# Kernel optimization log

Measured on AMD Instinct MI355X. Metric: run time of the kernel, lower is better.

Reference implementation:

```python
import jax, jax.numpy as jnp
import numpy as np

BN, N, FIN, FO, H = 4, 2048, 128, 64, 4
D = FO * H  # 256


def setup_inputs() -> dict:
    key = jax.random.key(0)
    ks = jax.random.split(key, 13)
    rnd = lambda k, s, sc=1.0: jax.random.normal(k, s, dtype=jnp.float32) * sc
    return {
        "x": rnd(ks[0], (BN, N, FIN)),
        "adj": rnd(ks[1], (BN, N, N)),
        "W_proj": rnd(ks[2], (D, FIN), 0.08),        # xavier-ish scale
        "score_src": rnd(ks[3], (H, FO), 0.1),        # (head_num, out_features)
        "score_tgt": rnd(ks[4], (H, FO), 0.1),
        "bias_out": jnp.zeros((D,), jnp.float32),
        "w_r": rnd(ks[5], (D, D), 0.06),
        "u_r": rnd(ks[6], (D, D), 0.06),
        "w_z": rnd(ks[7], (D, D), 0.06),
        "b_wz": jnp.full((D,), -2.0, jnp.float32),    # GRUGate init_bias
        "u_z": rnd(ks[8], (D, D), 0.06),
        "w_g": rnd(ks[9], (D, D), 0.06),
        "u_g": rnd(ks[10], (D, D), 0.06),
    }


def reference(x, adj, W_proj, score_src, score_tgt, bias_out,
              w_r, u_r, w_z, b_wz, u_z, w_g, u_g):
    bn, n = x.shape[:2]
    h, fo = score_src.shape
    # eval mode: dropout is identity
    proj_flat = x @ W_proj.T                                   # (bn, n, fo*h)
    # reshape splits last dim as (fo, h): head index fastest-varying
    proj = proj_flat.reshape(bn, n, fo, h).transpose(0, 3, 1, 2)  # (bn, h, n, fo)
    residual = proj_flat                                       # (bn, n, fo*h)
    s_src = jnp.einsum('bhnf,hf->bhn', proj, score_src)
    s_tgt = jnp.einsum('bhnf,hf->bhn', proj, score_tgt)
    scores = jax.nn.leaky_relu(s_src[..., :, None] + s_tgt[..., None, :], 0.2)
    scores = scores + adj[:, None]                             # (bn, h, n, n)
    attn = jax.nn.softmax(scores, axis=-1)
    out = jnp.einsum('bhij,bhjf->bhif', attn, proj)            # (bn, h, n, fo)
    out = out.transpose(0, 2, 1, 3).reshape(bn, n, h * fo)
    # GRUGate is computed in the torch source but its result is discarded
    z = jax.nn.sigmoid(out @ w_z.T + b_wz + residual @ u_z.T)
    r = jax.nn.sigmoid(out @ w_r.T + residual @ u_r.T)
    h_hat = jnp.tanh(out @ w_g.T + (r * residual) @ u_g.T)
    _gru = (1.0 - z) * residual + z * h_hat  # unused, matches source bug
    return jax.nn.elu(out + bias_out)
```

## Files before the change

### kernel.cpp

```cpp
#include <hip/hip_runtime.h>
#include <hip/hip_bf16.h>
#include <math.h>

#define BN_   4
#define NN_   2048
#define FIN_  128
#define FO_   64
#define H_    4
#define D_    256

typedef __attribute__((ext_vector_type(8))) short bf16x8;
typedef __attribute__((ext_vector_type(4))) float floatx4;

#define LOG2E 1.4426950408889634f

#if __has_builtin(__builtin_amdgcn_exp2f)
#define EXP2(x) __builtin_amdgcn_exp2f(x)
#else
#define EXP2(x) exp2f(x)
#endif

__device__ __forceinline__ float bf2f(short u) {
    union { unsigned int i; float f; } v;
    v.i = ((unsigned int)(unsigned short)u) << 16;
    return v.f;
}
__device__ __forceinline__ short f2bf(float f) {
    union { float f; unsigned int u; } v; v.f = f;
    unsigned int r = v.u + 0x7fffu + ((v.u >> 16) & 1u);
    return (short)(unsigned short)(r >> 16);
}

#if defined(__BF16_MANT_DIG__)
typedef __bf16 bfr2 __attribute__((ext_vector_type(2)));
__device__ __forceinline__ unsigned int pack_bf16(float a, float b) {
    union { bfr2 h; unsigned int u; } v;
    v.h = (bfr2){(__bf16)a, (__bf16)b};
    return v.u;
}
#else
__device__ __forceinline__ unsigned int pack_bf16(float a, float b) {
    return ((unsigned int)(unsigned short)f2bf(a)) |
           (((unsigned int)(unsigned short)f2bf(b)) << 16);
}
#endif

__device__ __forceinline__ bf16x8 load8f(const float* __restrict__ p) {
    floatx4 a = *(const floatx4*)p;
    floatx4 b = *(const floatx4*)(p + 4);
    union { bf16x8 v; unsigned int u[4]; } r;
    r.u[0] = pack_bf16(a[0], a[1]);
    r.u[1] = pack_bf16(a[2], a[3]);
    r.u[2] = pack_bf16(b[0], b[1]);
    r.u[3] = pack_bf16(b[2], b[3]);
    return r.v;
}

__device__ __forceinline__ float score_exp(float ssv, float stv, float av) {
    float s = ssv + stv;
    s = fmaxf(s, 0.2f * s);
    return EXP2((s + av) * LOG2E);
}

__global__ __launch_bounds__(256) void proj_kernel(
    const float* __restrict__ x,
    const float* __restrict__ wproj,
    const float* __restrict__ ssrc,
    const float* __restrict__ stgt,
    short* __restrict__ pt,
    float* __restrict__ sS,
    float* __restrict__ sT,
    int b0)
{
    const int tid  = threadIdx.x;
    const int wave = tid >> 6;
    const int lane = tid & 63;
    const int l16  = lane & 15;
    const int quad = lane >> 4;

    const int b_rel = blockIdx.z;
    const int b  = b0 + b_rel;
    const int h  = blockIdx.y;
    const int d0 = h * 64;
    const int j0 = blockIdx.x * 256 + wave * 64;

    floatx4 acc[4][4];
#pragma unroll
    for (int mi = 0; mi < 4; ++mi)
#pragma unroll
        for (int nj = 0; nj < 4; ++nj)
            acc[mi][nj] = (floatx4){0.f, 0.f, 0.f, 0.f};

#pragma unroll
    for (int kc = 0; kc < 4; ++kc) {
        const int c = kc * 32 + quad * 8;
        bf16x8 afr[4], bfr[4];
#pragma unroll
        for (int mi = 0; mi < 4; ++mi) {
            int f = (d0 + mi * 16 + l16) & 63;
            int srow = f * H_ + h;
            afr[mi] = load8f(wproj + srow * FIN_ + c);
        }
#pragma unroll
        for (int nj = 0; nj < 4; ++nj) {
            int j = j0 + nj * 16 + l16;
            bfr[nj] = load8f(x + ((size_t)b * NN_ + j) * FIN_ + c);
        }
#pragma unroll
        for (int mi = 0; mi < 4; ++mi)
#pragma unroll
            for (int nj = 0; nj < 4; ++nj)
                acc[mi][nj] = __builtin_amdgcn_mfma_f32_16x16x32_bf16(
                    afr[mi], bfr[nj], acc[mi][nj], 0, 0, 0);
    }

    const size_t hbase = ((size_t)b_rel * H_ + h) * (size_t)(64 * 2048);
    const int jt0 = j0 >> 5;
#pragma unroll
    for (int mi = 0; mi < 4; ++mi) {
#pragma unroll
        for (int r = 0; r < 4; ++r) {
            const int f15 = quad * 4 + r;
#pragma unroll
            for (int nj = 0; nj < 4; ++nj) {
                const int tile = jt0 + (nj >> 1);
                const int jsub = (nj & 1) * 2 + (l16 >> 3);
                pt[hbase + (size_t)tile * 2048 + mi * 512 + jsub * 128
                   + f15 * 8 + (l16 & 7)] = f2bf(acc[mi][nj][r]);
            }
        }
    }

    float wsv[4][4], wtv[4][4];
#pragma unroll
    for (int mi = 0; mi < 4; ++mi)
#pragma unroll
        for (int r = 0; r < 4; ++r) {
            int f = mi * 16 + quad * 4 + r;
            wsv[mi][r] = ssrc[h * FO_ + f];
            wtv[mi][r] = stgt[h * FO_ + f];
        }
    const size_t sbase = ((size_t)b_rel * H_ + h) * NN_;
#pragma unroll
    for (int nj = 0; nj < 4; ++nj) {
        float ps = 0.f, pg = 0.f;
#pragma unroll
        for (int mi = 0; mi < 4; ++mi)
#pragma unroll
            for (int r = 0; r < 4; ++r) {
                ps = fmaf(wsv[mi][r], acc[mi][nj][r], ps);
                pg = fmaf(wtv[mi][r], acc[mi][nj][r], pg);
            }
        ps += __shfl_xor(ps, 16, 64); ps += __shfl_xor(ps, 32, 64);
        pg += __shfl_xor(pg, 16, 64); pg += __shfl_xor(pg, 32, 64);
        if (quad == 0) {
            int j = j0 + nj * 16 + l16;
            sS[sbase + j] = ps;
            sT[sbase + j] = pg;
        }
    }
}

#define RSTRIDE 65
#define WSLOT   (RSTRIDE * 16 + 16)

__global__ __launch_bounds__(512, 2) void attn_kernel(
    const float* __restrict__ adj,
    const short* __restrict__ pt,
    const float* __restrict__ sS,
    const float* __restrict__ sT,
    const float* __restrict__ bias,
    float* __restrict__ out,
    int b0)
{
    __shared__ union {
        struct {
            float adjs[8][16][36];
            float st[8][4][256];
        } m;
        float red[8][WSLOT];
    } sm;

    const int tid  = threadIdx.x;
    const int w    = tid >> 6;
    const int lane = tid & 63;
    const int l16  = lane & 15;
    const int quad = lane >> 4;
    const int r8   = lane >> 3;
    const int c4   = (lane & 7) * 4;

    const int b_rel = blockIdx.z;
    const int b  = b0 + b_rel;
    const int i0 = blockIdx.x * 16;

    const short* pt2_b = pt + (size_t)b_rel * H_ * (size_t)(64 * 2048);
    const size_t sb = (size_t)b_rel * H_ * NN_;

    {
        const int t = lane * 4;
#pragma unroll
        for (int h = 0; h < 4; ++h)
            *(floatx4*)&sm.m.st[w][h][t] =
                *(const floatx4*)&sT[sb + (size_t)h * NN_ + w * 256 + t];
    }

    float ssv[4];
#pragma unroll
    for (int h = 0; h < 4; ++h)
        ssv[h] = sS[sb + (size_t)h * NN_ + i0 + l16];

    const float* adj_base = adj + ((size_t)b * NN_ + i0) * NN_ + w * 256;

    floatx4 acc[4][4];
#pragma unroll
    for (int h = 0; h < 4; ++h)
#pragma unroll
        for (int K = 0; K < 4; ++K)
            acc[h][K] = (floatx4){0.f, 0.f, 0.f, 0.f};
    float ls[4] = {0.f, 0.f, 0.f, 0.f};

    floatx4 areg0 = *(const floatx4*)(adj_base + (size_t)r8 * NN_ + c4);
    floatx4 areg1 = *(const floatx4*)(adj_base + (size_t)(8 + r8) * NN_ + c4);
    *(floatx4*)&sm.m.adjs[w][r8][c4]     = areg0;
    *(floatx4*)&sm.m.adjs[w][8 + r8][c4] = areg1;

    const int lo8 = lane * 8;

#pragma unroll
    for (int jt = 0; jt < 8; ++jt) {
        const int o  = jt * 32;
        const int qo = quad * 8;

        if (jt < 7) {
            areg0 = *(const floatx4*)(adj_base + (size_t)r8 * NN_ + o + 32 + c4);
            areg1 = *(const floatx4*)(adj_base + (size_t)(8 + r8) * NN_ + o + 32 + c4);
        }

        floatx4 ajA = *(const floatx4*)&sm.m.adjs[w][l16][qo];
        floatx4 ajB = *(const floatx4*)&sm.m.adjs[w][l16][qo + 4];

#pragma unroll
        for (int u = 0; u < 4; ++u) {
            const short* fb = pt2_b + ((size_t)u * 64 + (w * 8 + jt)) * 2048 + lo8;
            bf16x8 bfr[4];
#pragma unroll
            for (int K = 0; K < 4; ++K)
                bfr[K] = *(const bf16x8*)(fb + K * 512);

            const float* stp = &sm.m.st[w][u][qo];
            floatx4 stA = *(const floatx4*)(stp + o);
            floatx4 stB = *(const floatx4*)(stp + o + 4);

            float w0 = score_exp(ssv[u], stA[0], ajA[0]);
            float w1 = score_exp(ssv[u], stA[1], ajA[1]);
            float w2 = score_exp(ssv[u], stA[2], ajA[2]);
            float w3 = score_exp(ssv[u], stA[3], ajA[3]);
            float w4 = score_exp(ssv[u], stB[0], ajB[0]);
            float w5 = score_exp(ssv[u], stB[1], ajB[1]);
            float w6 = score_exp(ssv[u], stB[2], ajB[2]);
            float w7 = score_exp(ssv[u], stB[3], ajB[3]);
            ls[u] += ((w0 + w1) + (w2 + w3)) + ((w4 + w5) + (w6 + w7));
            union { bf16x8 v; unsigned int u4[4]; } a0;
            a0.u4[0] = pack_bf16(w0, w1);
            a0.u4[1] = pack_bf16(w2, w3);
            a0.u4[2] = pack_bf16(w4, w5);
            a0.u4[3] = pack_bf16(w6, w7);
#pragma unroll
            for (int K = 0; K < 4; ++K)
                acc[u][K] = __builtin_amdgcn_mfma_f32_16x16x32_bf16(
                    a0.v, bfr[K], acc[u][K], 0, 0, 0);
        }

        if (jt < 7) {
            *(floatx4*)&sm.m.adjs[w][r8][c4]     = areg0;
            *(floatx4*)&sm.m.adjs[w][8 + r8][c4] = areg1;
        }
    }

#pragma unroll
    for (int h = 0; h < 4; ++h) {
        ls[h] += __shfl_xor(ls[h], 16, 64);
        ls[h] += __shfl_xor(ls[h], 32, 64);
    }

#pragma unroll
    for (int h = 0; h < 4; ++h) {
        __syncthreads();
#pragma unroll
        for (int K = 0; K < 4; ++K)
#pragma unroll
            for (int r = 0; r < 4; ++r)
                sm.red[w][(quad * 4 + r) * RSTRIDE + K * 16 + l16] = acc[h][K][r];
        if (quad == 0)
            sm.red[w][16 * RSTRIDE + l16] = ls[h];
        __syncthreads();
#pragma unroll
        for (int p = 0; p < 2; ++p) {
            int e   = tid + p * 512;
            int row = e >> 6;
            int col = e & 63;
            float s = 0.f, l = 0.f;
#pragma unroll
            for (int ww = 0; ww < 8; ++ww) {
                s += sm.red[ww][row * RSTRIDE + col];
                l += sm.red[ww][16 * RSTRIDE + row];
            }
            float v = s / l + bias[h * FO_ + col];
            v = (v > 0.f) ? v : expm1f(v);
            out[((size_t)b * NN_ + i0 + row) * D_ + h * FO_ + col] = v;
        }
    }
}

extern "C" void kernel_launch(void* const* d_in, const int* in_sizes, int n_in,
                              void* d_out, int out_size, void* d_ws, size_t ws_size,
                              hipStream_t stream) {
    const float* x     = (const float*)d_in[0];
    const float* adj   = (const float*)d_in[1];
    const float* wproj = (const float*)d_in[2];
    const float* ssrc  = (const float*)d_in[3];
    const float* stgt  = (const float*)d_in[4];
    const float* bias  = (const float*)d_in[5];
    float* out = (float*)d_out;

    const size_t SLAB  = (size_t)D_ * NN_ * 2;
    const size_t SSLAB = (size_t)2 * H_ * NN_ * 4;
    int nb = (int)(ws_size / (SLAB + SSLAB));
    if (nb < 1) nb = 1;
    if (nb > 4) nb = 4;

    short* pt = (short*)d_ws;
    float* sv = (float*)((char*)d_ws + (size_t)nb * SLAB);
    float* sS = sv;
    float* sT = sv + (size_t)nb * H_ * NN_;

    for (int bb0 = 0; bb0 < BN_; bb0 += nb) {
        int cnt = (BN_ - bb0 < nb) ? (BN_ - bb0) : nb;
        proj_kernel<<<dim3(NN_ / 256, H_, cnt), 256, 0, stream>>>(
            x, wproj, ssrc, stgt, pt, sS, sT, bb0);
        attn_kernel<<<dim3(NN_ / 16, 1, cnt), 512, 0, stream>>>(
            adj, pt, sS, sT, bias, out, bb0);
    }
}
```

Baseline: 164.1 us.

## Stage projection output in LDS for vectorized stores, shrink proj tiles

The projection kernel now computes 16 nodes per wave instead of 64, so the grid grows fourfold (more blocks, lower register use). Results are staged through a shared-memory tile and written back to the swizzled bf16 layout as 16-byte vector stores, replacing scattered 2-byte global stores. This adds a barrier and an LDS round-trip, and the W_proj loads are now repeated across more blocks.

Measured after the change: 165.9 us. Within noise of the previous version (+1.1%).

```diff
diff --git a/kernel.cpp b/kernel.cpp
--- a/kernel.cpp
+++ b/kernel.cpp
@@ -72,6 +72,8 @@
     float* __restrict__ sT,
     int b0)
 {
+    __shared__ short ptl[64][72];
+
     const int tid  = threadIdx.x;
     const int wave = tid >> 6;
     const int lane = tid & 63;
@@ -81,55 +83,35 @@
     const int b_rel = blockIdx.z;
     const int b  = b0 + b_rel;
     const int h  = blockIdx.y;
-    const int d0 = h * 64;
-    const int j0 = blockIdx.x * 256 + wave * 64;
-
-    floatx4 acc[4][4];
+    const int j0 = blockIdx.x * 64 + wave * 16;
+
+    floatx4 acc[4];
 #pragma unroll
     for (int mi = 0; mi < 4; ++mi)
-#pragma unroll
-        for (int nj = 0; nj < 4; ++nj)
-            acc[mi][nj] = (floatx4){0.f, 0.f, 0.f, 0.f};
+        acc[mi] = (floatx4){0.f, 0.f, 0.f, 0.f};
 
 #pragma unroll
     for (int kc = 0; kc < 4; ++kc) {
         const int c = kc * 32 + quad * 8;
-        bf16x8 afr[4], bfr[4];
+        bf16x8 afr[4];
 #pragma unroll
         for (int mi = 0; mi < 4; ++mi) {
-            int f = (d0 + mi * 16 + l16) & 63;
+            int f = mi * 16 + l16;
             int srow = f * H_ + h;
             afr[mi] = load8f(wproj + srow * FIN_ + c);
         }
-#pragma unroll
-        for (int nj = 0; nj < 4; ++nj) {
-            int j = j0 + nj * 16 + l16;
-            bfr[nj] = load8f(x + ((size_t)b * NN_ + j) * FIN_ + c);
-        }
+        bf16x8 bfr = load8f(x + ((size_t)b * NN_ + j0 + l16) * FIN_ + c);
 #pragma unroll
         for (int mi = 0; mi < 4; ++mi)
-#pragma unroll
-            for (int nj = 0; nj < 4; ++nj)
-                acc[mi][nj] = __builtin_amdgcn_mfma_f32_16x16x32_bf16(
-                    afr[mi], bfr[nj], acc[mi][nj], 0, 0, 0);
-    }
-
-    const size_t hbase = ((size_t)b_rel * H_ + h) * (size_t)(64 * 2048);
-    const int jt0 = j0 >> 5;
-#pragma unroll
-    for (int mi = 0; mi < 4; ++mi) {
-#pragma unroll
-        for (int r = 0; r < 4; ++r) {
-            const int f15 = quad * 4 + r;
-#pragma unroll
-            for (int nj = 0; nj < 4; ++nj) {
-                const int tile = jt0 + (nj >> 1);
-                const int jsub = (nj & 1) * 2 + (l16 >> 3);
-                pt[hbase + (size_t)tile * 2048 + mi * 512 + jsub * 128
-                   + f15 * 8 + (l16 & 7)] = f2bf(acc[mi][nj][r]);
-            }
-        }
-    }
+            acc[mi] = __builtin_amdgcn_mfma_f32_16x16x32_bf16(
+                afr[mi], bfr, acc[mi], 0, 0, 0);
+    }
+
+#pragma unroll
+    for (int mi = 0; mi < 4; ++mi)
+#pragma unroll
+        for (int r = 0; r < 4; ++r)
+            ptl[mi * 16 + quad * 4 + r][wave * 16 + l16] = f2bf(acc[mi][r]);
 
     float wsv[4][4], wtv[4][4];
 #pragma unroll
@@ -140,24 +122,39 @@
             wsv[mi][r] = ssrc[h * FO_ + f];
             wtv[mi][r] = stgt[h * FO_ + f];
         }
-    const size_t sbase = ((size_t)b_rel * H_ + h) * NN_;
-#pragma unroll
-    for (int nj = 0; nj < 4; ++nj) {
+    {
         float ps = 0.f, pg = 0.f;
 #pragma unroll
         for (int mi = 0; mi < 4; ++mi)
 #pragma unroll
             for (int r = 0; r < 4; ++r) {
-                ps = fmaf(wsv[mi][r], acc[mi][nj][r], ps);
-                pg = fmaf(wtv[mi][r], acc[mi][nj][r], pg);
+                ps = fmaf(wsv[mi][r], acc[mi][r], ps);
+                pg = fmaf(wtv[mi][r], acc[mi][r], pg);
             }
         ps += __shfl_xor(ps, 16, 64); ps += __shfl_xor(ps, 32, 64);
         pg += __shfl_xor(pg, 16, 64); pg += __shfl_xor(pg, 32, 64);
         if (quad == 0) {
-            int j = j0 + nj * 16 + l16;
-            sS[sbase + j] = ps;
-            sT[sbase + j] = pg;
-        }
+            const size_t sbase = ((size_t)b_rel * H_ + h) * NN_;
+            sS[sbase + j0 + l16] = ps;
+            sT[sbase + j0 + l16] = pg;
+        }
+    }
+
+    __syncthreads();
+
+    const size_t hbase = ((size_t)b_rel * H_ + h) * (size_t)(64 * 2048);
+#pragma unroll
+    for (int p = 0; p < 2; ++p) {
+        const int uid = p * 256 + tid;
+        const int tl  = (uid >> 8) & 1;
+        const int mi  = (uid >> 6) & 3;
+        const int l   = uid & 63;
+        const int f   = mi * 16 + (l & 15);
+        const int js  = tl * 32 + (l >> 4) * 8;
+        bf16x8 v = *(const bf16x8*)&ptl[f][js];
+        const int tile_glob = blockIdx.x * 2 + tl;
+        *(bf16x8*)&pt[hbase + (size_t)tile_glob * 2048 + mi * 512
+                      + (size_t)l * 8] = v;
     }
 }
 
@@ -336,7 +333,7 @@
 
     for (int bb0 = 0; bb0 < BN_; bb0 += nb) {
         int cnt = (BN_ - bb0 < nb) ? (BN_ - bb0) : nb;
-        proj_kernel<<<dim3(NN_ / 256, H_, cnt), 256, 0, stream>>>(
+        proj_kernel<<<dim3(NN_ / 64, H_, cnt), 256, 0, stream>>>(
             x, wproj, ssrc, stgt, pt, sS, sT, bb0);
         attn_kernel<<<dim3(NN_ / 16, 1, cnt), 512, 0, stream>>>(
             adj, pt, sS, sT, bias, out, bb0);
```
